# Optimization experiments

Hardware: AMD Instinct MI355X
Metric: run time of the kernel (lower is better)

Reference implementation:

```python
import jax, jax.numpy as jnp
import numpy as np

COMPRESS_RATIO = 4
HEAD_DIM = 512
COFF = 2  # overlap (compress_ratio == 4) doubles the projection width
EPS = 1e-6


def setup_inputs() -> dict:
    key = jax.random.key(0)
    k1, k2, k3, k4 = jax.random.split(key, 4)
    B, S, D = 4, 4096, 4096
    OD = COFF * HEAD_DIM  # 1024
    scale = 1.0 / np.sqrt(D)
    return {
        "x": jax.random.normal(k1, (B, S, D), dtype=jnp.float32),
        "wkv_w": jax.random.normal(k2, (OD, D), dtype=jnp.float32) * scale,
        "wgate_w": jax.random.normal(k3, (OD, D), dtype=jnp.float32) * scale,
        "ape": jax.random.normal(k4, (COMPRESS_RATIO, OD), dtype=jnp.float32) * 0.02,
        "norm_w": jnp.ones((HEAD_DIM,), dtype=jnp.float32),
    }


def reference(x, wkv_w, wgate_w, ape, norm_w):
    # x: [B, S, D]; windowed KV compression (NSA-style):
    # gated projection -> per-position learned abs pos embed -> window pool -> RMSNorm
    B, S, D = x.shape
    r = COMPRESS_RATIO
    nW = S // r
    kv = jnp.einsum("bsd,od->bso", x, wkv_w)          # [B, S, coff*hd]
    gate = jax.nn.sigmoid(jnp.einsum("bsd,od->bso", x, wgate_w))
    kv = kv * gate
    # add learned absolute position embedding per position-within-window
    kv = kv + jnp.tile(ape, (nW, 1))                    # [S, coff*hd] broadcast over B
    # pool each window of r tokens; split overlap streams into separate tokens
    kv = kv.reshape(B, nW, r, COFF, HEAD_DIM).mean(axis=2)  # [B, nW, coff, hd]
    kv = kv.reshape(B, nW * COFF, HEAD_DIM)                 # [B, 2*nW, hd]
    # RMSNorm over head_dim
    var = jnp.mean(kv * kv, axis=-1, keepdims=True)
    return norm_w * kv * jax.lax.rsqrt(var + EPS)
```

## Files before the change

kernel.cpp:

```cpp
#include <hip/hip_runtime.h>
#include <hip/hip_bf16.h>

#define D_DIM 4096
#define OD    1024
#define M_TOT 16384
#define N_TOT 2048
#define BM 256
#define BN 256
#define BK 64

#define GLOBAL_AS __attribute__((address_space(1)))
#define LDS_AS    __attribute__((address_space(3)))

typedef __attribute__((ext_vector_type(8))) short          bf16x8;
typedef __attribute__((ext_vector_type(8))) unsigned short u16x8;
typedef __attribute__((ext_vector_type(4))) float          f32x4;

__device__ __forceinline__ unsigned short f2bf(float f) {
    unsigned int u = __float_as_uint(f);
    u = (u + 0x7fffu + ((u >> 16) & 1u)) >> 16;
    return (unsigned short)u;
}

__device__ __forceinline__ float sigm(float x) {
    return 1.0f / (1.0f + __expf(-x));
}

__device__ __forceinline__ void gload16(const void* g, void* l) {
    __builtin_amdgcn_global_load_lds((const GLOBAL_AS void*)g, (LDS_AS void*)l, 16, 0, 0);
}

__global__ void prep_weights(const float* __restrict__ wkv,
                             const float* __restrict__ wgate,
                             unsigned short* __restrict__ Wc) {
    int t  = blockIdx.x * 256 + threadIdx.x;
    int n  = t >> 9;
    int k8 = t & 511;
    const float* src = (n & 1) ? wgate : wkv;
    const float4* s4 = (const float4*)(src + (size_t)(n >> 1) * D_DIM + k8 * 8);
    float4 a = s4[0], b = s4[1];
    u16x8 o;
    o[0] = f2bf(a.x); o[1] = f2bf(a.y); o[2] = f2bf(a.z); o[3] = f2bf(a.w);
    o[4] = f2bf(b.x); o[5] = f2bf(b.y); o[6] = f2bf(b.z); o[7] = f2bf(b.w);
    *(u16x8*)(Wc + (size_t)n * D_DIM + k8 * 8) = o;
}

__global__ void prep_x(const float* __restrict__ x, unsigned short* __restrict__ xb) {
    size_t t = (size_t)blockIdx.x * 256 + threadIdx.x;
    const float4* s = (const float4*)(x + t * 8);
    float4 a = s[0], b = s[1];
    u16x8 o;
    o[0] = f2bf(a.x); o[1] = f2bf(a.y); o[2] = f2bf(a.z); o[3] = f2bf(a.w);
    o[4] = f2bf(b.x); o[5] = f2bf(b.y); o[6] = f2bf(b.z); o[7] = f2bf(b.w);
    *(u16x8*)(xb + t * 8) = o;
}

__global__ void prep_ape(const float* __restrict__ ape, float* __restrict__ am) {
    int t = blockIdx.x * 256 + threadIdx.x;
    if (t < OD)
        am[t] = 0.25f * (ape[t] + ape[OD + t] + ape[2 * OD + t] + ape[3 * OD + t]);
}

extern __shared__ __align__(16) unsigned short smem_u16[];

__global__ __launch_bounds__(512)
void gemm_fused_8ph(const unsigned short* __restrict__ A,
                    const unsigned short* __restrict__ Wc,
                    const float* __restrict__ ape_mean,
                    float* __restrict__ out_pooled) {
    unsigned short* Asb[2] = {smem_u16,             smem_u16 + BM * BK};
    unsigned short* Bsb[2] = {smem_u16 + 2 * BM * BK, smem_u16 + 3 * BM * BK};

    const int tid  = threadIdx.x;
    const int lane = tid & 63;
    const int wave = tid >> 6;
    const int wm   = wave >> 2;
    const int wn   = wave & 3;
    const int h    = lane & 15;
    const int q    = lane >> 4;

    const int bid = blockIdx.x;
    const int j   = bid >> 3;
    const int m0  = ((bid & 7) * 8 + (j >> 3)) * BM;
    const int n0  = (j & 7) * BN;

    const int sc8 = (lane & 7) ^ ((lane >> 3) & 7);
    const unsigned short* Ag = A  + (size_t)(m0 + wave * 8 + (lane >> 3)) * D_DIM + sc8 * 8;
    const unsigned short* Bg = Wc + (size_t)(n0 + (wave & 3) * 8 + (lane >> 3)) * D_DIM + sc8 * 8;
    const int bstripe = wave >> 2;

#define STAGE_A(buf, half, kofs)                                                   \
    do {                                                                           \
        gload16(Ag + (size_t)((half) * 64) * D_DIM + (kofs),                       \
                Asb[buf] + ((half) * 64 + wave * 8) * BK);                         \
        gload16(Ag + (size_t)((half) * 64 + 128) * D_DIM + (kofs),                 \
                Asb[buf] + ((half) * 64 + 128 + wave * 8) * BK);                   \
    } while (0)

#define STAGE_B(buf, qb, kofs)                                                     \
    do {                                                                           \
        const int r0_ = (qb) * 32 + bstripe * 64;                                  \
        const int r1_ = (qb) * 32 + (2 + bstripe) * 64;                            \
        gload16(Bg + (size_t)r0_ * D_DIM + (kofs),                                 \
                Bsb[buf] + (r0_ + (wave & 3) * 8) * BK);                           \
        gload16(Bg + (size_t)r1_ * D_DIM + (kofs),                                 \
                Bsb[buf] + (r1_ + (wave & 3) * 8) * BK);                           \
    } while (0)

#define PHASE(buf, qa, qb, STAGECODE, VM)                                          \
    do {                                                                           \
        bf16x8 av[4][2], bv[2][2];                                                 \
        _Pragma("unroll")                                                          \
        for (int mi = 0; mi < 4; ++mi) {                                           \
            const int row = wm * 128 + ((qa) * 4 + mi) * 16 + h;                   \
            _Pragma("unroll")                                                      \
            for (int ks = 0; ks < 2; ++ks)                                         \
                av[mi][ks] = *(const bf16x8*)&Asb[buf][(row * BK + ks * 32 +       \
                             q * 8) ^ ((row & 7) << 3)];                           \
        }                                                                          \
        _Pragma("unroll")                                                          \
        for (int ni = 0; ni < 2; ++ni) {                                           \
            const int rw = wn * 64 + ((qb) * 2 + ni) * 16 + h;                     \
            _Pragma("unroll")                                                      \
            for (int ks = 0; ks < 2; ++ks)                                         \
                bv[ni][ks] = *(const bf16x8*)&Bsb[buf][(rw * BK + ks * 32 +        \
                             q * 8) ^ ((rw & 7) << 3)];                            \
        }                                                                          \
        STAGECODE;                                                                 \
        if (VM) asm volatile("s_waitcnt vmcnt(4)" ::: "memory");                   \
        __builtin_amdgcn_s_barrier();                                              \
        __builtin_amdgcn_s_setprio(1);                                             \
        _Pragma("unroll")                                                          \
        for (int mi = 0; mi < 4; ++mi)                                             \
            _Pragma("unroll")                                                      \
            for (int ni = 0; ni < 2; ++ni)                                         \
                _Pragma("unroll")                                                  \
                for (int ks = 0; ks < 2; ++ks)                                     \
                    acc[(qa) * 4 + mi][(qb) * 2 + ni] =                            \
                        __builtin_amdgcn_mfma_f32_16x16x32_bf16(                   \
                            av[mi][ks], bv[ni][ks],                                \
                            acc[(qa) * 4 + mi][(qb) * 2 + ni], 0, 0, 0);           \
        __builtin_amdgcn_s_setprio(0);                                             \
        __builtin_amdgcn_s_barrier();                                              \
    } while (0)

    f32x4 acc[8][4];
    const f32x4 z = {0.f, 0.f, 0.f, 0.f};
#pragma unroll
    for (int i = 0; i < 8; ++i)
#pragma unroll
        for (int jj = 0; jj < 4; ++jj) acc[i][jj] = z;

    STAGE_A(0, 0, 0); STAGE_A(0, 1, 0); STAGE_B(0, 0, 0); STAGE_B(0, 1, 0);
    STAGE_B(1, 0, 64); STAGE_A(1, 0, 64);
    asm volatile("s_waitcnt vmcnt(4)" ::: "memory");
    __builtin_amdgcn_s_barrier();

    for (int kt2 = 0; kt2 < D_DIM; kt2 += 2 * BK) {
        const int kb1 = kt2 + BK;
        const int kna = (kt2 + 2 * BK) & 4095;
        const int knb = (kt2 + 3 * BK) & 4095;
        PHASE(0, 0, 0, STAGE_A(1, 1, kb1), 0);
        PHASE(0, 1, 0, STAGE_B(1, 1, kb1), 0);
        PHASE(0, 0, 1, STAGE_B(0, 0, kna), 0);
        PHASE(0, 1, 1, STAGE_A(0, 0, kna), 1);
        PHASE(1, 0, 0, STAGE_A(0, 1, kna), 0);
        PHASE(1, 1, 0, STAGE_B(0, 1, kna), 0);
        PHASE(1, 0, 1, STAGE_B(1, 0, knb), 0);
        PHASE(1, 1, 1, STAGE_A(1, 0, knb), 1);
    }
#undef STAGE_A
#undef STAGE_B
#undef PHASE

    const bool is_kv = ((h & 1) == 0);
#pragma unroll
    for (int mi = 0; mi < 8; ++mi) {
        const int mbase = m0 + wm * 128 + mi * 16 + q * 4;
        const int wglob = mbase >> 2;
#pragma unroll
        for (int ni = 0; ni < 4; ++ni) {
            f32x4 kv = acc[mi][ni];
            float g0 = __shfl_xor(kv[0], 1);
            float g1 = __shfl_xor(kv[1], 1);
            float g2 = __shfl_xor(kv[2], 1);
            float g3 = __shfl_xor(kv[3], 1);
            if (is_kv) {
                float s = kv[0] * sigm(g0) + kv[1] * sigm(g1) +
                          kv[2] * sigm(g2) + kv[3] * sigm(g3);
                int n = n0 + wn * 64 + ni * 16 + h;
                int o = n >> 1;
                out_pooled[(size_t)wglob * OD + o] = 0.25f * s + ape_mean[o];
            }
        }
    }
}

__global__ __launch_bounds__(256)
void gemm_fused_f32(const float* __restrict__ Aptr,
                    const unsigned short* __restrict__ Wc,
                    const float* __restrict__ ape_mean,
                    float* __restrict__ out_pooled) {
    __shared__ __align__(16) unsigned short As[128 * BK];
    __shared__ __align__(16) unsigned short Bs[128 * BK];
    const int tid  = threadIdx.x;
    const int lane = tid & 63;
    const int wave = tid >> 6;
    const int wr   = wave >> 1;
    const int wc   = wave & 1;
    const int n0   = blockIdx.x * 128;
    const int m0   = blockIdx.y * 128;
    const int h    = lane & 15;
    const int q    = lane >> 4;

    f32x4 acc[4][4];
    const f32x4 z = {0.f, 0.f, 0.f, 0.f};
#pragma unroll
    for (int i = 0; i < 4; ++i)
#pragma unroll
        for (int jj = 0; jj < 4; ++jj) acc[i][jj] = z;

    for (int kt = 0; kt < D_DIM; kt += BK) {
#pragma unroll
        for (int i = 0; i < 4; ++i) {
            int chunk = tid + i * 256;
            int row = chunk >> 3, c8 = chunk & 7;
            int dst = (row * BK + c8 * 8) ^ ((row & 7) << 3);
            const float4* s = (const float4*)(Aptr + (size_t)(m0 + row) * D_DIM + kt + c8 * 8);
            float4 a = s[0], b = s[1];
            u16x8 o;
            o[0] = f2bf(a.x); o[1] = f2bf(a.y); o[2] = f2bf(a.z); o[3] = f2bf(a.w);
            o[4] = f2bf(b.x); o[5] = f2bf(b.y); o[6] = f2bf(b.z); o[7] = f2bf(b.w);
            *(u16x8*)&As[dst] = o;
        }
#pragma unroll
        for (int i = 0; i < 4; ++i) {
            int chunk = tid + i * 256;
            int row = chunk >> 3, c8 = chunk & 7;
            int dst = (row * BK + c8 * 8) ^ ((row & 7) << 3);
            *(u16x8*)&Bs[dst] =
                *(const u16x8*)(Wc + (size_t)(n0 + row) * D_DIM + kt + c8 * 8);
        }
        __syncthreads();
#pragma unroll
        for (int ks = 0; ks < 2; ++ks) {
            const int kb = ks * 32 + q * 8;
            bf16x8 af[4], bfr[4];
#pragma unroll
            for (int am = 0; am < 4; ++am) {
                int row = wr * 64 + am * 16 + h;
                af[am] = *(const bf16x8*)&As[(row * BK + kb) ^ ((row & 7) << 3)];
            }
#pragma unroll
            for (int bn = 0; bn < 4; ++bn) {
                int row = wc * 64 + bn * 16 + h;
                bfr[bn] = *(const bf16x8*)&Bs[(row * BK + kb) ^ ((row & 7) << 3)];
            }
#pragma unroll
            for (int am = 0; am < 4; ++am)
#pragma unroll
                for (int bn = 0; bn < 4; ++bn)
                    acc[am][bn] = __builtin_amdgcn_mfma_f32_16x16x32_bf16(
                        af[am], bfr[bn], acc[am][bn], 0, 0, 0);
        }
        __syncthreads();
    }
    const bool is_kv = ((h & 1) == 0);
#pragma unroll
    for (int am = 0; am < 4; ++am) {
        const int mbase = m0 + wr * 64 + am * 16 + q * 4;
        const int wglob = mbase >> 2;
#pragma unroll
        for (int bn = 0; bn < 4; ++bn) {
            f32x4 kv = acc[am][bn];
            float g0 = __shfl_xor(kv[0], 1);
            float g1 = __shfl_xor(kv[1], 1);
            float g2 = __shfl_xor(kv[2], 1);
            float g3 = __shfl_xor(kv[3], 1);
            if (is_kv) {
                float s = kv[0] * sigm(g0) + kv[1] * sigm(g1) +
                          kv[2] * sigm(g2) + kv[3] * sigm(g3);
                int n = n0 + wc * 64 + bn * 16 + h;
                int o = n >> 1;
                out_pooled[(size_t)wglob * OD + o] = 0.25f * s + ape_mean[o];
            }
        }
    }
}

__global__ void rmsnorm_inplace(float* __restrict__ out, const float* __restrict__ nw) {
    int token = blockIdx.x * 4 + (threadIdx.x >> 6);
    int lane  = threadIdx.x & 63;
    float4* p = (float4*)(out + (size_t)token * 512);
    float4 v0 = p[lane * 2], v1 = p[lane * 2 + 1];
    float ss = v0.x * v0.x + v0.y * v0.y + v0.z * v0.z + v0.w * v0.w +
               v1.x * v1.x + v1.y * v1.y + v1.z * v1.z + v1.w * v1.w;
#pragma unroll
    for (int off = 32; off > 0; off >>= 1) ss += __shfl_xor(ss, off);
    float rs = rsqrtf(ss * (1.0f / 512.0f) + 1e-6f);
    const float4* w4 = (const float4*)nw;
    float4 w0 = w4[lane * 2], w1 = w4[lane * 2 + 1];
    float4 r0, r1;
    r0.x = v0.x * rs * w0.x; r0.y = v0.y * rs * w0.y;
    r0.z = v0.z * rs * w0.z; r0.w = v0.w * rs * w0.w;
    r1.x = v1.x * rs * w1.x; r1.y = v1.y * rs * w1.y;
    r1.z = v1.z * rs * w1.z; r1.w = v1.w * rs * w1.w;
    p[lane * 2]     = r0;
    p[lane * 2 + 1] = r1;
}

extern "C" void kernel_launch(void* const* d_in, const int* in_sizes, int n_in,
                              void* d_out, int out_size, void* d_ws, size_t ws_size,
                              hipStream_t stream) {
    const float* x     = (const float*)d_in[0];
    const float* wkv   = (const float*)d_in[1];
    const float* wgate = (const float*)d_in[2];
    const float* ape   = (const float*)d_in[3];
    const float* normw = (const float*)d_in[4];
    float* out = (float*)d_out;

    unsigned short* Wc  = (unsigned short*)d_ws;
    float* ape_mean     = (float*)((char*)d_ws + (size_t)16 * 1024 * 1024);
    unsigned short* xb  = (unsigned short*)((char*)d_ws + (size_t)16 * 1024 * 1024 + 65536);
    const size_t need_xb = (size_t)16 * 1024 * 1024 + 65536 + (size_t)M_TOT * D_DIM * 2;
    const bool use_xb = (ws_size >= need_xb);

    prep_weights<<<4096, 256, 0, stream>>>(wkv, wgate, Wc);
    prep_ape<<<4, 256, 0, stream>>>(ape, ape_mean);

    if (use_xb) {
        prep_x<<<32768, 256, 0, stream>>>(x, xb);
        (void)hipFuncSetAttribute(
            reinterpret_cast<const void*>(&gemm_fused_8ph),
            hipFuncAttributeMaxDynamicSharedMemorySize, 131072);
        gemm_fused_8ph<<<(M_TOT / BM) * (N_TOT / BN), 512, 131072, stream>>>(
            xb, Wc, ape_mean, out);
    } else {
        gemm_fused_f32<<<dim3(N_TOT / 128, M_TOT / 128), 256, 0, stream>>>(
            x, Wc, ape_mean, out);
    }

    rmsnorm_inplace<<<2048, 256, 0, stream>>>(out, normw);
}
```

Baseline: 330.8 us.

## Restructure GEMM main loop from eight to four phases per k-pair

Merges pairs of pipeline phases so each phase reads a full 4x4 MFMA sub-tile set from LDS and issues 32 MFMAs. This halves the number of barriers per k-iteration and regroups the global-to-LDS stage loads around the new phases, with the vmcnt waits retuned to match. It also adds a min-blocks-per-CU hint of 2 to launch_bounds. That hint tightens the register budget while the 128-float accumulator plus larger operand fragments are live, which risks spills. The 128 KB LDS per block likely prevents two blocks per CU anyway.

```diff
diff --git a/kernel.cpp b/kernel.cpp
--- a/kernel.cpp
+++ b/kernel.cpp
@@ -63,12 +63,12 @@
 
 extern __shared__ __align__(16) unsigned short smem_u16[];
 
-__global__ __launch_bounds__(512)
-void gemm_fused_8ph(const unsigned short* __restrict__ A,
+__global__ __launch_bounds__(512, 2)
+void gemm_fused_4ph(const unsigned short* __restrict__ A,
                     const unsigned short* __restrict__ Wc,
                     const float* __restrict__ ape_mean,
                     float* __restrict__ out_pooled) {
-    unsigned short* Asb[2] = {smem_u16,             smem_u16 + BM * BK};
+    unsigned short* Asb[2] = {smem_u16,               smem_u16 + BM * BK};
     unsigned short* Bsb[2] = {smem_u16 + 2 * BM * BK, smem_u16 + 3 * BM * BK};
 
     const int tid  = threadIdx.x;
@@ -107,9 +107,12 @@
                 Bsb[buf] + (r1_ + (wave & 3) * 8) * BK);                           \
     } while (0)
 
-#define PHASE(buf, qa, qb, STAGECODE, VM)                                          \
+#define BAR() __builtin_amdgcn_s_barrier()
+#define VMW2() asm volatile("s_waitcnt vmcnt(2)" ::: "memory")
+
+#define PHASE(buf, qa, STAGECODE, VM)                                              \
     do {                                                                           \
-        bf16x8 av[4][2], bv[2][2];                                                 \
+        bf16x8 av[4][2], bv[4][2];                                                 \
         _Pragma("unroll")                                                          \
         for (int mi = 0; mi < 4; ++mi) {                                           \
             const int row = wm * 128 + ((qa) * 4 + mi) * 16 + h;                   \
@@ -119,29 +122,29 @@
                              q * 8) ^ ((row & 7) << 3)];                           \
         }                                                                          \
         _Pragma("unroll")                                                          \
-        for (int ni = 0; ni < 2; ++ni) {                                           \
-            const int rw = wn * 64 + ((qb) * 2 + ni) * 16 + h;                     \
+        for (int ni = 0; ni < 4; ++ni) {                                           \
+            const int rw = wn * 64 + ni * 16 + h;                                  \
             _Pragma("unroll")                                                      \
             for (int ks = 0; ks < 2; ++ks)                                         \
                 bv[ni][ks] = *(const bf16x8*)&Bsb[buf][(rw * BK + ks * 32 +        \
                              q * 8) ^ ((rw & 7) << 3)];                            \
         }                                                                          \
         STAGECODE;                                                                 \
-        if (VM) asm volatile("s_waitcnt vmcnt(4)" ::: "memory");                   \
-        __builtin_amdgcn_s_barrier();                                              \
+        if (VM) VMW2();                                                            \
+        BAR();                                                                     \
         __builtin_amdgcn_s_setprio(1);                                             \
         _Pragma("unroll")                                                          \
         for (int mi = 0; mi < 4; ++mi)                                             \
             _Pragma("unroll")                                                      \
-            for (int ni = 0; ni < 2; ++ni)                                         \
+            for (int ni = 0; ni < 4; ++ni)                                         \
                 _Pragma("unroll")                                                  \
                 for (int ks = 0; ks < 2; ++ks)                                     \
-                    acc[(qa) * 4 + mi][(qb) * 2 + ni] =                            \
+                    acc[(qa) * 4 + mi][ni] =                                       \
                         __builtin_amdgcn_mfma_f32_16x16x32_bf16(                   \
                             av[mi][ks], bv[ni][ks],                                \
-                            acc[(qa) * 4 + mi][(qb) * 2 + ni], 0, 0, 0);           \
+                            acc[(qa) * 4 + mi][ni], 0, 0, 0);                      \
         __builtin_amdgcn_s_setprio(0);                                             \
-        __builtin_amdgcn_s_barrier();                                              \
+        BAR();                                                                     \
     } while (0)
 
     f32x4 acc[8][4];
@@ -152,26 +155,24 @@
         for (int jj = 0; jj < 4; ++jj) acc[i][jj] = z;
 
     STAGE_A(0, 0, 0); STAGE_A(0, 1, 0); STAGE_B(0, 0, 0); STAGE_B(0, 1, 0);
-    STAGE_B(1, 0, 64); STAGE_A(1, 0, 64);
-    asm volatile("s_waitcnt vmcnt(4)" ::: "memory");
-    __builtin_amdgcn_s_barrier();
+    STAGE_A(1, 0, 64);
+    VMW2();
+    BAR();
 
     for (int kt2 = 0; kt2 < D_DIM; kt2 += 2 * BK) {
         const int kb1 = kt2 + BK;
         const int kna = (kt2 + 2 * BK) & 4095;
         const int knb = (kt2 + 3 * BK) & 4095;
-        PHASE(0, 0, 0, STAGE_A(1, 1, kb1), 0);
-        PHASE(0, 1, 0, STAGE_B(1, 1, kb1), 0);
-        PHASE(0, 0, 1, STAGE_B(0, 0, kna), 0);
-        PHASE(0, 1, 1, STAGE_A(0, 0, kna), 1);
-        PHASE(1, 0, 0, STAGE_A(0, 1, kna), 0);
-        PHASE(1, 1, 0, STAGE_B(0, 1, kna), 0);
-        PHASE(1, 0, 1, STAGE_B(1, 0, knb), 0);
-        PHASE(1, 1, 1, STAGE_A(1, 0, knb), 1);
+        PHASE(0, 0, { STAGE_A(1, 1, kb1); STAGE_B(1, 0, kb1); STAGE_B(1, 1, kb1); }, 0);
+        PHASE(0, 1, { STAGE_A(0, 0, kna); }, 1);
+        PHASE(1, 0, { STAGE_A(0, 1, kna); STAGE_B(0, 0, kna); }, 0);
+        PHASE(1, 1, { STAGE_B(0, 1, kna); STAGE_A(1, 0, knb); }, 1);
     }
 #undef STAGE_A
 #undef STAGE_B
 #undef PHASE
+#undef BAR
+#undef VMW2
 
     const bool is_kv = ((h & 1) == 0);
 #pragma unroll
@@ -331,9 +332,9 @@
     if (use_xb) {
         prep_x<<<32768, 256, 0, stream>>>(x, xb);
         (void)hipFuncSetAttribute(
-            reinterpret_cast<const void*>(&gemm_fused_8ph),
+            reinterpret_cast<const void*>(&gemm_fused_4ph),
             hipFuncAttributeMaxDynamicSharedMemorySize, 131072);
-        gemm_fused_8ph<<<(M_TOT / BM) * (N_TOT / BN), 512, 131072, stream>>>(
+        gemm_fused_4ph<<<(M_TOT / BM) * (N_TOT / BN), 512, 131072, stream>>>(
             xb, Wc, ape_mean, out);
     } else {
         gemm_fused_f32<<<dim3(N_TOT / 128, M_TOT / 128), 256, 0, stream>>>(
```

Measured after the change: 460.1 us (median of 2 runs). 39.1% more time.
